# Performance work log

Measured on AMD Instinct MI355X. Metric: run time of the kernel, lower is better.

The kernel has to match this reference:

```python
import jax, jax.numpy as jnp
import numpy as np

N, E, B = 20000, 320000, 64
NODE_DIM, HID, HEADS, L, EMB = 128, 256, 4, 3, 256
C = HID // HEADS
NEG_SLOPE = 0.2
LN_EPS = 1e-5


def setup_inputs() -> dict:
    key = jax.random.key(0)
    ks = jax.random.split(key, 12)
    inp = {
        'x': jax.random.normal(ks[0], (N, NODE_DIM), jnp.float32),
        'edge_index': jax.random.randint(ks[1], (2, E), 0, N, jnp.int32),
        'batch': ((jnp.arange(N, dtype=jnp.int32) * B) // N).astype(jnp.int32),
        'W_in': jax.random.normal(ks[2], (NODE_DIM, HID), jnp.float32) * 0.05,
        'b_in': jnp.zeros((HID,), jnp.float32),
        'cls_token': jax.random.normal(ks[3], (HID,), jnp.float32),
        'W_gat': jax.random.normal(ks[4], (L, HID, HID), jnp.float32) * 0.05,
        'att_src': jax.random.normal(ks[5], (L, HEADS, C), jnp.float32) * 0.1,
        'att_dst': jax.random.normal(ks[6], (L, HEADS, C), jnp.float32) * 0.1,
        'b_gat': jnp.zeros((L, HID), jnp.float32),
        'ln_g': jnp.ones((L, HID), jnp.float32),
        'ln_b': jnp.zeros((L, HID), jnp.float32),
        'W_out': jax.random.normal(ks[7], (HID, EMB), jnp.float32) * 0.05,
        'b_out': jnp.zeros((EMB,), jnp.float32),
    }
    return inp


def _layer_norm(h, g, b):
    mu = jnp.mean(h, axis=-1, keepdims=True)
    var = jnp.mean(jnp.square(h - mu), axis=-1, keepdims=True)
    return (h - mu) * jax.lax.rsqrt(var + LN_EPS) * g + b


def _gat_layer(h, src, dst, n_nodes, W, a_s, a_d, bias):
    # PyG GATConv: shared linear, per-head attention, softmax over incoming edges
    xs = (h @ W).reshape(n_nodes, HEADS, C)          # (N',H,C)
    al_s = jnp.sum(xs * a_s, axis=-1)                # (N',H)
    al_d = jnp.sum(xs * a_d, axis=-1)                # (N',H)
    e = jax.nn.leaky_relu(al_s[src] + al_d[dst], NEG_SLOPE)  # (E',H)
    m = jax.ops.segment_max(e, dst, num_segments=n_nodes)
    ex = jnp.exp(e - m[dst])
    den = jax.ops.segment_sum(ex, dst, num_segments=n_nodes)
    alpha = ex / (den[dst] + 1e-16)                  # (E',H)
    msg = alpha[:, :, None] * xs[src]                # (E',H,C)
    out = jax.ops.segment_sum(msg, dst, num_segments=n_nodes)
    return out.reshape(n_nodes, HID) + bias


def reference(x, edge_index, batch, W_in, b_in, cls_token, W_gat, att_src,
              att_dst, b_gat, ln_g, ln_b, W_out, b_out):
    n_new = B + N
    h = x @ W_in + b_in                              # (N,HID)
    cls = jnp.broadcast_to(cls_token[None, :], (B, HID))
    h = jnp.concatenate([cls, h], axis=0)            # (B+N,HID)
    # build augmented edge list: shifted edges + bidirectional CLS edges + self loops
    src0 = edge_index[0] + B
    dst0 = edge_index[1] + B
    node_idx = jnp.arange(N, dtype=jnp.int32) + B
    cls_idx = batch
    loops = jnp.arange(n_new, dtype=jnp.int32)
    src = jnp.concatenate([src0, cls_idx, node_idx, loops])
    dst = jnp.concatenate([dst0, node_idx, cls_idx, loops])
    for l in range(L):
        g = _gat_layer(h, src, dst, n_new, W_gat[l], att_src[l], att_dst[l], b_gat[l])
        h = _layer_norm(h + g, ln_g[l], ln_b[l])
    z_e = h[:B] @ W_out + b_out                      # (B,EMB)
    return z_e
```

## Files before the change

kernel.cpp:

```cpp
#include <hip/hip_runtime.h>
#include <hip/hip_bf16.h>

constexpr int HID = 256;
constexpr int CAP = 64;
constexpr float NEG = 0.2f;
constexpr float EPS = 1e-5f;

typedef __attribute__((ext_vector_type(8))) short bf16x8;
typedef __attribute__((ext_vector_type(4))) float f32x4;

static __device__ __forceinline__ unsigned short f2bf(float f) {
    unsigned u = __builtin_bit_cast(unsigned, f);
    u += 0x7fffu + ((u >> 16) & 1u);
    return (unsigned short)(u >> 16);
}
static __device__ __forceinline__ float bf2f(unsigned short h) {
    return __builtin_bit_cast(float, ((unsigned)h) << 16);
}
static __device__ __forceinline__ float elk(float v) {
    v = v > 0.f ? v : NEG * v;
    return __expf(v);
}


__device__ __forceinline__ void frag_task(const float* __restrict__ W,
                                          ushort* __restrict__ out,
                                          int KS, int nmat, int q) {
    int per = KS * 1024;
    if (q >= per * nmat) return;
    int mat = q / per, r = q - mat * per;
    int l = r & 63, nf = (r >> 6) & 15, kk = r >> 10;
    const float* Wm = W + (size_t)mat * KS * 32 * 256;
    int kb = kk * 32 + ((l >> 4) << 3);
    int col = nf * 16 + (l & 15);
    bf16x8 v;
#pragma unroll
    for (int j = 0; j < 8; ++j) v[j] = (short)f2bf(Wm[(size_t)(kb + j) * 256 + col]);
    *(bf16x8*)(out + (size_t)q * 8) = v;
}

__global__ void k_pre(const float* __restrict__ x, ushort* __restrict__ xb,
                      const float* __restrict__ cls, ushort* __restrict__ h0,
                      const float* __restrict__ W_in, ushort* __restrict__ wf_in,
                      const float* __restrict__ W_gat, ushort* __restrict__ wf_gat,
                      const int* __restrict__ batch, int* lo, int* hi,
                      int* cursor, int* csr, int N, int B, int n_new) {
    int bid = blockIdx.x, t = threadIdx.x;
    const int nb_cvt  = (N * 128 / 4 + 255) / 256;
    const int nb_init = (n_new + 255) / 256;
    const int nb_csr  = (n_new * CAP + 255) / 256;
    const int nb_bnd  = (N + 255) / 256;
    const int nb_cls  = (B * HID / 4 + 255) / 256;
    const int nb_fin  = (4 * 1024 + 255) / 256;

    if (bid < nb_cvt) {
        int i = bid * 256 + t;
        int n4 = N * 128 / 4;
        if (i < n4) {
            float4 v = ((const float4*)x)[i];
            ushort4 o;
            o.x = f2bf(v.x); o.y = f2bf(v.y); o.z = f2bf(v.z); o.w = f2bf(v.w);
            ((ushort4*)xb)[i] = o;
        }
        return;
    }
    bid -= nb_cvt;
    if (bid < nb_init) {
        int i = bid * 256 + t;
        if (i < n_new) cursor[i] = 0;
        return;
    }
    bid -= nb_init;
    if (bid < nb_csr) {
        int i = bid * 256 + t;
        if (i < n_new * CAP) csr[i] = -1;
        return;
    }
    bid -= nb_csr;
    if (bid < nb_bnd) {
        int i = bid * 256 + t;
        if (i < N) {
            int b = batch[i];
            if (i == 0 || batch[i - 1] != b) lo[b] = i;
            if (i == N - 1 || batch[i + 1] != b) hi[b] = i + 1;
        }
        return;
    }
    bid -= nb_bnd;
    if (bid < nb_cls) {
        int i = bid * 256 + t;
        if (i < B * HID / 4) {
            int ch = (i & 63) * 4;
            ushort4 o;
            o.x = f2bf(cls[ch]); o.y = f2bf(cls[ch + 1]);
            o.z = f2bf(cls[ch + 2]); o.w = f2bf(cls[ch + 3]);
            ((ushort4*)h0)[i] = o;
        }
        return;
    }
    bid -= nb_cls;
    if (bid < nb_fin) {
        frag_task(W_in, wf_in, 4, 1, bid * 256 + t);
        return;
    }
    bid -= nb_fin;
    frag_task(W_gat, wf_gat, 8, 3, bid * 256 + t);
}


__global__ void k_fill(const int* __restrict__ src0, const int* __restrict__ dst0,
                       int* cursor, int* __restrict__ csr, int E, int B) {
    int e = blockIdx.x * blockDim.x + threadIdx.x;
    if (e < E) {
        int d = dst0[e] + B;
        int p = atomicAdd(&cursor[d], 1);
        if (p < CAP) csr[d * CAP + p] = src0[e] + B;
    }
}


__global__ void k_alpha(const int* __restrict__ csr, const int* __restrict__ cursor,
                        const float* __restrict__ als, const float* __restrict__ ald,
                        const int* __restrict__ batch,
                        float* __restrict__ a4T, float* __restrict__ acls,
                        float* __restrict__ aself, float* __restrict__ aclsinT,
                        int n_new, int B) {
    const int NSLOT = n_new * CAP;
    int i = blockIdx.x * 256 + threadIdx.x;
    if (i < NSLOT) {
        int d = i >> 6, p = i & (CAP - 1);
        int deg = cursor[d];
        deg = deg < CAP ? deg : CAP;
        int degp = (deg + 7) & ~7;
        if (p >= degp) return;
        int s = csr[i];
        float ox = 0.f, oy = 0.f, oz = 0.f, ow = 0.f;
        if (s >= 0) {
            float4 s4 = ((const float4*)als)[s];
            float4 d4 = ((const float4*)ald)[d];
            ox = elk(s4.x + d4.x);
            oy = elk(s4.y + d4.y);
            oz = elk(s4.z + d4.z);
            ow = elk(s4.w + d4.w);
        }
        a4T[i] = ox;
        a4T[(size_t)NSLOT + i] = oy;
        a4T[(size_t)2 * NSLOT + i] = oz;
        a4T[(size_t)3 * NSLOT + i] = ow;
        return;
    }
    int n = i - NSLOT;
    if (n < n_new) {
        float4 d4 = ((const float4*)ald)[n];
        float4 s4 = ((const float4*)als)[n];
        float4 o;
        o.x = elk(s4.x + d4.x);
        o.y = elk(s4.y + d4.y);
        o.z = elk(s4.z + d4.z);
        o.w = elk(s4.w + d4.w);
        ((float4*)aself)[n] = o;
        if (n >= B) {
            int c = batch[n - B];
            float4 cs = ((const float4*)als)[c];
            float4 p4;
            p4.x = elk(cs.x + d4.x);
            p4.y = elk(cs.y + d4.y);
            p4.z = elk(cs.z + d4.z);
            p4.w = elk(cs.w + d4.w);
            ((float4*)acls)[n] = p4;
            float4 cd = ((const float4*)ald)[c];
            aclsinT[n] = elk(s4.x + cd.x);
            aclsinT[(size_t)n_new + n] = elk(s4.y + cd.y);
            aclsinT[(size_t)2 * n_new + n] = elk(s4.z + cd.z);
            aclsinT[(size_t)3 * n_new + n] = elk(s4.w + cd.w);
        }
    }
}


template <int KS, bool ATT, bool BIAS>
__global__ __launch_bounds__(256, 4) void k_mgemm(
    const ushort* __restrict__ A, const ushort* __restrict__ Wf,
    const float* __restrict__ bias, ushort* __restrict__ outb,
    const float* __restrict__ att_s, const float* __restrict__ att_d,
    float* __restrict__ al_s, float* __restrict__ al_d, int rows)
{
    constexpr int K = KS * 32;
    int lane = threadIdx.x & 63, w = threadIdx.x >> 6;
    int rbase = blockIdx.x * 32;
    int arow0 = rbase + (lane & 15);
    int kofs = (lane >> 4) << 3;

    f32x4 acc[2][4];
#pragma unroll
    for (int mf = 0; mf < 2; ++mf)
#pragma unroll
        for (int nf = 0; nf < 4; ++nf) acc[mf][nf] = (f32x4){0.f, 0.f, 0.f, 0.f};

    const ushort* a0p = A + (size_t)arow0 * K + kofs;
    const ushort* a1p = a0p + (size_t)16 * K;
    bool g0 = arow0 < rows, g1 = (arow0 + 16) < rows;

#pragma unroll
    for (int kk = 0; kk < KS; ++kk) {
        bf16x8 af0 = {0, 0, 0, 0, 0, 0, 0, 0}, af1 = {0, 0, 0, 0, 0, 0, 0, 0};
        if (g0) af0 = *(const bf16x8*)(a0p + kk * 32);
        if (g1) af1 = *(const bf16x8*)(a1p + kk * 32);
        const bf16x8* wp = ((const bf16x8*)Wf) + (size_t)(kk * 16 + 4 * w) * 64 + lane;
#pragma unroll
        for (int nf = 0; nf < 4; ++nf) {
            bf16x8 bv = wp[nf * 64];
            acc[0][nf] = __builtin_amdgcn_mfma_f32_16x16x32_bf16(af0, bv, acc[0][nf], 0, 0, 0);
            acc[1][nf] = __builtin_amdgcn_mfma_f32_16x16x32_bf16(af1, bv, acc[1][nf], 0, 0, 0);
        }
    }

    int rg = (lane >> 4) * 4;
    int c0 = lane & 15;
    int colbase = w * 64;
    float bv[4];
    if (BIAS) {
#pragma unroll
        for (int nf = 0; nf < 4; ++nf) bv[nf] = bias[colbase + nf * 16 + c0];
    }
#pragma unroll
    for (int mf = 0; mf < 2; ++mf)
#pragma unroll
        for (int r = 0; r < 4; ++r) {
            int row = rbase + mf * 16 + rg + r;
            if (row < rows) {
#pragma unroll
                for (int nf = 0; nf < 4; ++nf) {
                    float v = acc[mf][nf][r];
                    if (BIAS) v += bv[nf];
                    outb[(size_t)row * HID + colbase + nf * 16 + c0] = f2bf(v);
                }
            }
        }

    if (ATT) {
        float as[4], ad[4];
#pragma unroll
        for (int nf = 0; nf < 4; ++nf) {
            as[nf] = att_s[colbase + nf * 16 + c0];
            ad[nf] = att_d[colbase + nf * 16 + c0];
        }
#pragma unroll
        for (int mf = 0; mf < 2; ++mf)
#pragma unroll
            for (int r = 0; r < 4; ++r) {
                float ps = 0.f, pd = 0.f;
#pragma unroll
                for (int nf = 0; nf < 4; ++nf) {
                    float v = acc[mf][nf][r];
                    ps += v * as[nf];
                    pd += v * ad[nf];
                }
#pragma unroll
                for (int o = 1; o < 16; o <<= 1) {
                    ps += __shfl_xor(ps, o, 64);
                    pd += __shfl_xor(pd, o, 64);
                }
                int row = rbase + mf * 16 + rg + r;
                if (c0 == 0 && row < rows) {
                    al_s[row * 4 + w] = ps;
                    al_d[row * 4 + w] = pd;
                }
            }
    }
}


__global__ __launch_bounds__(256, 4) void k_agg(
    const ushort* __restrict__ hb, const ushort* __restrict__ xs,
    const float* __restrict__ a4T, const float* __restrict__ acls,
    const float* __restrict__ aself, const float* __restrict__ aclsinT,
    const int* __restrict__ cursor, const int* __restrict__ csr,
    const int* __restrict__ batch, const int* __restrict__ lo,
    const int* __restrict__ hi,
    const float* __restrict__ b_gat, const float* __restrict__ ln_g,
    const float* __restrict__ ln_b,
    ushort* __restrict__ h_out, int n_new, int B)
{
    int t = threadIdx.x, w = t >> 6, lane = t & 63;
    int n = blockIdx.x * 4 + w;
    if (n >= n_new) return;
    int es = lane >> 5, cg = lane & 31, head = cg >> 3;
    const int NSLOT = n_new * CAP;

    float acc[8] = {0.f, 0.f, 0.f, 0.f, 0.f, 0.f, 0.f, 0.f};
    float den = 0.f;

    if (n >= B) {
        int gdeg = cursor[n];
        gdeg = gdeg < CAP ? gdeg : CAP;
        int gdegp = (gdeg + 7) & ~7;
        int clssrc = batch[n - B];
        bf16x8 xcls  = *((const bf16x8*)(xs + (size_t)clssrc * HID) + cg);
        bf16x8 xself = *((const bf16x8*)(xs + (size_t)n * HID) + cg);
        float acl = acls[n * 4 + head];
        float asf = aself[n * 4 + head];

        const int4* cp = (const int4*)(csr + n * CAP);
        const float4* ap = (const float4*)(a4T + (size_t)head * NSLOT + (size_t)n * CAP);
#pragma unroll 2
        for (int eb = 0; eb < gdegp; eb += 8) {
            int idx = (eb >> 2) + es;
            int4 s4 = cp[idx];
            float4 av = ap[idx];
            int s0 = s4.x < 0 ? 0 : s4.x;
            int s1 = s4.y < 0 ? 0 : s4.y;
            int s2 = s4.z < 0 ? 0 : s4.z;
            int s3 = s4.w < 0 ? 0 : s4.w;
            bf16x8 x0 = *((const bf16x8*)(xs + (size_t)s0 * HID) + cg);
            bf16x8 x1 = *((const bf16x8*)(xs + (size_t)s1 * HID) + cg);
            bf16x8 x2 = *((const bf16x8*)(xs + (size_t)s2 * HID) + cg);
            bf16x8 x3 = *((const bf16x8*)(xs + (size_t)s3 * HID) + cg);
            den += av.x + av.y + av.z + av.w;
#pragma unroll
            for (int j = 0; j < 8; ++j) {
                acc[j] += av.x * bf2f((unsigned short)x0[j]);
                acc[j] += av.y * bf2f((unsigned short)x1[j]);
                acc[j] += av.z * bf2f((unsigned short)x2[j]);
                acc[j] += av.w * bf2f((unsigned short)x3[j]);
            }
        }
        if (es == 0) {
            den += acl + asf;
#pragma unroll
            for (int j = 0; j < 8; ++j)
                acc[j] += acl * bf2f((unsigned short)xcls[j]) +
                          asf * bf2f((unsigned short)xself[j]);
        }
    } else {
        int cb = B + lo[n], cdeg = hi[n] - lo[n];
        bf16x8 xself = *((const bf16x8*)(xs + (size_t)n * HID) + cg);
        float asf = aself[n * 4 + head];
        const float* wp = aclsinT + (size_t)head * n_new;
        for (int eb = 0; eb < cdeg; eb += 8) {
            int b0 = eb + es * 4;
#pragma unroll
            for (int k = 0; k < 4; ++k) {
                int e = b0 + k;
                int ec = e < cdeg ? e : cdeg - 1;
                int src = cb + ec;
                float a = e < cdeg ? wp[src] : 0.f;
                bf16x8 xv = *((const bf16x8*)(xs + (size_t)src * HID) + cg);
                den += a;
#pragma unroll
                for (int j = 0; j < 8; ++j) acc[j] += a * bf2f((unsigned short)xv[j]);
            }
        }
        if (es == 0) {
            den += asf;
#pragma unroll
            for (int j = 0; j < 8; ++j) acc[j] += asf * bf2f((unsigned short)xself[j]);
        }
    }

#pragma unroll
    for (int j = 0; j < 8; ++j) acc[j] += __shfl_xor(acc[j], 32, 64);
    den += __shfl_xor(den, 32, 64);
    float inv = 1.f / (den + 1e-16f);

    bf16x8 hv = *((const bf16x8*)(hb + (size_t)n * HID) + cg);
    const float4* bgp = (const float4*)(b_gat + cg * 8);
    float4 bg0 = bgp[0], bg1 = bgp[1];
    float bg[8] = {bg0.x, bg0.y, bg0.z, bg0.w, bg1.x, bg1.y, bg1.z, bg1.w};
    float r[8];
#pragma unroll
    for (int j = 0; j < 8; ++j)
        r[j] = bf2f((unsigned short)hv[j]) + acc[j] * inv + bg[j];

    float ss = 0.f;
#pragma unroll
    for (int j = 0; j < 8; ++j) ss += r[j];
#pragma unroll
    for (int o = 1; o < 32; o <<= 1) ss += __shfl_xor(ss, o, 64);
    float mu = ss * (1.f / HID);
    float vv = 0.f;
#pragma unroll
    for (int j = 0; j < 8; ++j) { r[j] -= mu; vv += r[j] * r[j]; }
#pragma unroll
    for (int o = 1; o < 32; o <<= 1) vv += __shfl_xor(vv, o, 64);
    float rs = rsqrtf(vv * (1.f / HID) + EPS);

    if (es == 0) {
        const float4* gp = (const float4*)(ln_g + cg * 8);
        const float4* bp = (const float4*)(ln_b + cg * 8);
        float4 g0 = gp[0], g1 = gp[1];
        float4 lb0 = bp[0], lb1 = bp[1];
        float gg[8] = {g0.x, g0.y, g0.z, g0.w, g1.x, g1.y, g1.z, g1.w};
        float bb[8] = {lb0.x, lb0.y, lb0.z, lb0.w, lb1.x, lb1.y, lb1.z, lb1.w};
        bf16x8 o8;
#pragma unroll
        for (int j = 0; j < 8; ++j) o8[j] = (short)f2bf(r[j] * rs * gg[j] + bb[j]);
        *((bf16x8*)(h_out + (size_t)n * HID) + cg) = o8;
    }
}


__global__ __launch_bounds__(256) void k_clsfused(
    const ushort* __restrict__ hb, const ushort* __restrict__ xs,
    const float* __restrict__ als, const float* __restrict__ ald,
    const int* __restrict__ lo, const int* __restrict__ hi,
    const float* __restrict__ b_gat, const float* __restrict__ ln_g,
    const float* __restrict__ ln_b,
    const float* __restrict__ W_out, const float* __restrict__ b_out,
    float* __restrict__ z, int n_new, int B)
{
    __shared__ float sacc[4][256];
    __shared__ float sden[4][4];
    __shared__ float red[8];
    __shared__ float hs[256];
    int b = blockIdx.x;
    int t = threadIdx.x, w = t >> 6, lane = t & 63;
    int es = lane >> 5, cg = lane & 31, head = cg >> 3;

    int cb = B + lo[b], cdeg = hi[b] - lo[b];
    float ald_h = ald[b * 4 + head];

    float acc[8] = {0.f, 0.f, 0.f, 0.f, 0.f, 0.f, 0.f, 0.f};
    float den = 0.f;
    for (int eb = w * 8; eb < cdeg; eb += 32) {
        int b0 = eb + es * 4;
#pragma unroll
        for (int k = 0; k < 4; ++k) {
            int e = b0 + k;
            int ec = e < cdeg ? e : cdeg - 1;
            int src = cb + ec;
            float a = e < cdeg ? elk(als[src * 4 + head] + ald_h) : 0.f;
            bf16x8 xv = *((const bf16x8*)(xs + (size_t)src * HID) + cg);
            den += a;
#pragma unroll
            for (int j = 0; j < 8; ++j) acc[j] += a * bf2f((unsigned short)xv[j]);
        }
    }
#pragma unroll
    for (int j = 0; j < 8; ++j) acc[j] += __shfl_xor(acc[j], 32, 64);
    den += __shfl_xor(den, 32, 64);
    if (es == 0) {
#pragma unroll
        for (int j = 0; j < 8; ++j) sacc[w][cg * 8 + j] = acc[j];
        if ((cg & 7) == 0) sden[w][head] = den;
    }
    __syncthreads();

    int c = t, hh = c >> 6;
    float atot = sacc[0][c] + sacc[1][c] + sacc[2][c] + sacc[3][c];
    float dtot = sden[0][hh] + sden[1][hh] + sden[2][hh] + sden[3][hh];
    float asf = elk(als[b * 4 + hh] + ald[b * 4 + hh]);
    atot += asf * bf2f(xs[(size_t)b * HID + c]);
    dtot += asf;
    float r = bf2f(hb[(size_t)b * HID + c]) + atot / (dtot + 1e-16f) + b_gat[c];

    float s1 = r;
#pragma unroll
    for (int o = 32; o > 0; o >>= 1) s1 += __shfl_xor(s1, o, 64);
    if (lane == 0) red[w] = s1;
    __syncthreads();
    float mu = (red[0] + red[1] + red[2] + red[3]) * (1.f / HID);
    float d = r - mu;
    float v2 = d * d;
#pragma unroll
    for (int o = 32; o > 0; o >>= 1) v2 += __shfl_xor(v2, o, 64);
    if (lane == 0) red[4 + w] = v2;
    __syncthreads();
    float var = (red[4] + red[5] + red[6] + red[7]) * (1.f / HID);
    float rs = rsqrtf(var + EPS);
    hs[c] = d * rs * ln_g[c] + ln_b[c];
    __syncthreads();

    float o = b_out[t];
#pragma unroll 8
    for (int k = 0; k < HID; ++k) o += hs[k] * W_out[k * HID + t];
    z[(size_t)b * HID + t] = o;
}


extern "C" void kernel_launch(void* const* d_in, const int* in_sizes, int n_in,
                              void* d_out, int out_size, void* d_ws, size_t ws_size,
                              hipStream_t stream) {
    const float* x      = (const float*)d_in[0];
    const int*   ei     = (const int*)d_in[1];
    const int*   batch  = (const int*)d_in[2];
    const float* W_in   = (const float*)d_in[3];
    const float* b_in   = (const float*)d_in[4];
    const float* cls    = (const float*)d_in[5];
    const float* W_gat  = (const float*)d_in[6];
    const float* att_s  = (const float*)d_in[7];
    const float* att_d  = (const float*)d_in[8];
    const float* b_gat  = (const float*)d_in[9];
    const float* ln_g   = (const float*)d_in[10];
    const float* ln_b   = (const float*)d_in[11];
    const float* W_out  = (const float*)d_in[12];
    const float* b_out  = (const float*)d_in[13];

    const int N = in_sizes[0] / 128;
    const int E = in_sizes[1] / 2;
    const int B = 64;
    const int n_new = N + B;
    const int* src0 = ei;
    const int* dst0 = ei + E;

    char* p = (char*)d_ws;
    auto alloc = [&](size_t bytes) -> void* {
        void* r = (void*)p;
        p += (bytes + 255) & ~(size_t)255;
        return r;
    };
    int*    cursor = (int*)alloc((size_t)n_new * 4);
    int*    csr    = (int*)alloc((size_t)n_new * CAP * 4);
    int*    lo     = (int*)alloc((size_t)B * 4);
    int*    hi     = (int*)alloc((size_t)B * 4);
    ushort* xb     = (ushort*)alloc((size_t)N * 128 * 2);
    ushort* h0b    = (ushort*)alloc((size_t)n_new * HID * 2);
    ushort* h1b    = (ushort*)alloc((size_t)n_new * HID * 2);
    ushort* xsb    = (ushort*)alloc((size_t)n_new * HID * 2);
    float*  als    = (float*)alloc((size_t)n_new * 4 * 4);
    float*  aldv   = (float*)alloc((size_t)n_new * 4 * 4);
    float*  a4T    = (float*)alloc((size_t)n_new * CAP * 4 * 4);
    float*  acls   = (float*)alloc((size_t)n_new * 4 * 4);
    float*  aselfv = (float*)alloc((size_t)n_new * 4 * 4);
    float*  aclsinT= (float*)alloc((size_t)n_new * 4 * 4);
    ushort* wf_in  = (ushort*)alloc((size_t)4 * 1024 * 8 * 2);
    ushort* wf_gat = (ushort*)alloc((size_t)3 * 8 * 1024 * 8 * 2);

    const int nb_pre = (N * 128 / 4 + 255) / 256 + (n_new + 255) / 256 +
                       (n_new * CAP + 255) / 256 + (N + 255) / 256 +
                       (B * HID / 4 + 255) / 256 +
                       (4 * 1024 + 255) / 256 + (3 * 8 * 1024 + 255) / 256;
    k_pre<<<nb_pre, 256, 0, stream>>>(x, xb, cls, h0b, W_in, wf_in, W_gat, wf_gat,
                                      batch, lo, hi, cursor, csr, N, B, n_new);
    k_fill<<<(E + 255) / 256, 256, 0, stream>>>(src0, dst0, cursor, csr, E, B);

    k_mgemm<4, false, true><<<(N + 31) / 32, 256, 0, stream>>>(
        xb, wf_in, b_in, h0b + (size_t)B * HID, nullptr, nullptr, nullptr, nullptr, N);

    const int nb_alpha = (n_new * CAP + n_new + 255) / 256;
    ushort* cur = h0b;
    ushort* nxt = h1b;
    for (int l = 0; l < 2; ++l) {
        k_mgemm<8, true, false><<<(n_new + 31) / 32, 256, 0, stream>>>(
            cur, wf_gat + (size_t)l * 65536, nullptr, xsb,
            att_s + l * HID, att_d + l * HID, als, aldv, n_new);
        k_alpha<<<nb_alpha, 256, 0, stream>>>(
            csr, cursor, als, aldv, batch, a4T, acls, aselfv, aclsinT, n_new, B);
        k_agg<<<(n_new + 3) / 4, 256, 0, stream>>>(
            cur, xsb, a4T, acls, aselfv, aclsinT, cursor, csr, batch, lo, hi,
            b_gat + l * HID, ln_g + l * HID, ln_b + l * HID, nxt, n_new, B);
        ushort* tmp = cur; cur = nxt; nxt = tmp;
    }
    k_mgemm<8, true, false><<<(n_new + 31) / 32, 256, 0, stream>>>(
        cur, wf_gat + (size_t)2 * 65536, nullptr, xsb,
        att_s + 2 * HID, att_d + 2 * HID, als, aldv, n_new);
    k_clsfused<<<B, 256, 0, stream>>>(
        cur, xsb, als, aldv, lo, hi,
        b_gat + 2 * HID, ln_g + 2 * HID, ln_b + 2 * HID,
        W_out, b_out, (float*)d_out, n_new, B);
}
```

Baseline: 195.7 us.

## Fuse attention-coefficient computation into aggregation kernel and drop alpha buffers

Removes the separate k_alpha kernel and its large per-slot a4T buffer, plus the acls, aself and aclsinT buffers. Edge attention weights are now computed inside k_agg. Each wave stages its node's neighbour coefficients in a per-wave LDS array, and the CLS, self and CLS-incoming coefficients are computed inline. This avoids writing and re-reading tens of MB of coefficients per layer and saves one launch per layer. In exchange, k_agg does redundant exponentials on the CLS path, and correctness relies on LDS visibility within a single wave without a barrier.

```diff
diff --git a/kernel.cpp b/kernel.cpp
--- a/kernel.cpp
+++ b/kernel.cpp
@@ -119,65 +119,6 @@
 }
 
 
-__global__ void k_alpha(const int* __restrict__ csr, const int* __restrict__ cursor,
-                        const float* __restrict__ als, const float* __restrict__ ald,
-                        const int* __restrict__ batch,
-                        float* __restrict__ a4T, float* __restrict__ acls,
-                        float* __restrict__ aself, float* __restrict__ aclsinT,
-                        int n_new, int B) {
-    const int NSLOT = n_new * CAP;
-    int i = blockIdx.x * 256 + threadIdx.x;
-    if (i < NSLOT) {
-        int d = i >> 6, p = i & (CAP - 1);
-        int deg = cursor[d];
-        deg = deg < CAP ? deg : CAP;
-        int degp = (deg + 7) & ~7;
-        if (p >= degp) return;
-        int s = csr[i];
-        float ox = 0.f, oy = 0.f, oz = 0.f, ow = 0.f;
-        if (s >= 0) {
-            float4 s4 = ((const float4*)als)[s];
-            float4 d4 = ((const float4*)ald)[d];
-            ox = elk(s4.x + d4.x);
-            oy = elk(s4.y + d4.y);
-            oz = elk(s4.z + d4.z);
-            ow = elk(s4.w + d4.w);
-        }
-        a4T[i] = ox;
-        a4T[(size_t)NSLOT + i] = oy;
-        a4T[(size_t)2 * NSLOT + i] = oz;
-        a4T[(size_t)3 * NSLOT + i] = ow;
-        return;
-    }
-    int n = i - NSLOT;
-    if (n < n_new) {
-        float4 d4 = ((const float4*)ald)[n];
-        float4 s4 = ((const float4*)als)[n];
-        float4 o;
-        o.x = elk(s4.x + d4.x);
-        o.y = elk(s4.y + d4.y);
-        o.z = elk(s4.z + d4.z);
-        o.w = elk(s4.w + d4.w);
-        ((float4*)aself)[n] = o;
-        if (n >= B) {
-            int c = batch[n - B];
-            float4 cs = ((const float4*)als)[c];
-            float4 p4;
-            p4.x = elk(cs.x + d4.x);
-            p4.y = elk(cs.y + d4.y);
-            p4.z = elk(cs.z + d4.z);
-            p4.w = elk(cs.w + d4.w);
-            ((float4*)acls)[n] = p4;
-            float4 cd = ((const float4*)ald)[c];
-            aclsinT[n] = elk(s4.x + cd.x);
-            aclsinT[(size_t)n_new + n] = elk(s4.y + cd.y);
-            aclsinT[(size_t)2 * n_new + n] = elk(s4.z + cd.z);
-            aclsinT[(size_t)3 * n_new + n] = elk(s4.w + cd.w);
-        }
-    }
-}
-
-
 template <int KS, bool ATT, bool BIAS>
 __global__ __launch_bounds__(256, 4) void k_mgemm(
     const ushort* __restrict__ A, const ushort* __restrict__ Wf,
@@ -273,8 +214,7 @@
 
 __global__ __launch_bounds__(256, 4) void k_agg(
     const ushort* __restrict__ hb, const ushort* __restrict__ xs,
-    const float* __restrict__ a4T, const float* __restrict__ acls,
-    const float* __restrict__ aself, const float* __restrict__ aclsinT,
+    const float* __restrict__ als, const float* __restrict__ ald,
     const int* __restrict__ cursor, const int* __restrict__ csr,
     const int* __restrict__ batch, const int* __restrict__ lo,
     const int* __restrict__ hi,
@@ -282,11 +222,11 @@
     const float* __restrict__ ln_b,
     ushort* __restrict__ h_out, int n_new, int B)
 {
+    __shared__ float s_a[4][4][68];
     int t = threadIdx.x, w = t >> 6, lane = t & 63;
     int n = blockIdx.x * 4 + w;
     if (n >= n_new) return;
     int es = lane >> 5, cg = lane & 31, head = cg >> 3;
-    const int NSLOT = n_new * CAP;
 
     float acc[8] = {0.f, 0.f, 0.f, 0.f, 0.f, 0.f, 0.f, 0.f};
     float den = 0.f;
@@ -295,19 +235,33 @@
         int gdeg = cursor[n];
         gdeg = gdeg < CAP ? gdeg : CAP;
         int gdegp = (gdeg + 7) & ~7;
+        float4 ald4 = ((const float4*)ald)[n];
+        float ald_h = head == 0 ? ald4.x : head == 1 ? ald4.y : head == 2 ? ald4.z : ald4.w;
+
+        {
+            bool v = lane < gdeg;
+            int s = v ? csr[n * CAP + lane] : 0;
+            float4 sa = {0.f, 0.f, 0.f, 0.f};
+            if (v) sa = ((const float4*)als)[s];
+            s_a[w][0][lane] = v ? elk(sa.x + ald4.x) : 0.f;
+            s_a[w][1][lane] = v ? elk(sa.y + ald4.y) : 0.f;
+            s_a[w][2][lane] = v ? elk(sa.z + ald4.z) : 0.f;
+            s_a[w][3][lane] = v ? elk(sa.w + ald4.w) : 0.f;
+        }
+
         int clssrc = batch[n - B];
         bf16x8 xcls  = *((const bf16x8*)(xs + (size_t)clssrc * HID) + cg);
         bf16x8 xself = *((const bf16x8*)(xs + (size_t)n * HID) + cg);
-        float acl = acls[n * 4 + head];
-        float asf = aself[n * 4 + head];
+        float acl = elk(als[clssrc * 4 + head] + ald_h);
+        float asf = elk(als[n * 4 + head] + ald_h);
 
         const int4* cp = (const int4*)(csr + n * CAP);
-        const float4* ap = (const float4*)(a4T + (size_t)head * NSLOT + (size_t)n * CAP);
+        const float* apl = &s_a[w][head][0];
 #pragma unroll 2
         for (int eb = 0; eb < gdegp; eb += 8) {
             int idx = (eb >> 2) + es;
             int4 s4 = cp[idx];
-            float4 av = ap[idx];
+            float4 av = *(const float4*)(apl + idx * 4);
             int s0 = s4.x < 0 ? 0 : s4.x;
             int s1 = s4.y < 0 ? 0 : s4.y;
             int s2 = s4.z < 0 ? 0 : s4.z;
@@ -334,9 +288,9 @@
         }
     } else {
         int cb = B + lo[n], cdeg = hi[n] - lo[n];
+        float ald_h = ald[n * 4 + head];
         bf16x8 xself = *((const bf16x8*)(xs + (size_t)n * HID) + cg);
-        float asf = aself[n * 4 + head];
-        const float* wp = aclsinT + (size_t)head * n_new;
+        float asf = elk(als[n * 4 + head] + ald_h);
         for (int eb = 0; eb < cdeg; eb += 8) {
             int b0 = eb + es * 4;
 #pragma unroll
@@ -344,7 +298,7 @@
                 int e = b0 + k;
                 int ec = e < cdeg ? e : cdeg - 1;
                 int src = cb + ec;
-                float a = e < cdeg ? wp[src] : 0.f;
+                float a = e < cdeg ? elk(als[src * 4 + head] + ald_h) : 0.f;
                 bf16x8 xv = *((const bf16x8*)(xs + (size_t)src * HID) + cg);
                 den += a;
 #pragma unroll
@@ -519,10 +473,6 @@
     ushort* xsb    = (ushort*)alloc((size_t)n_new * HID * 2);
     float*  als    = (float*)alloc((size_t)n_new * 4 * 4);
     float*  aldv   = (float*)alloc((size_t)n_new * 4 * 4);
-    float*  a4T    = (float*)alloc((size_t)n_new * CAP * 4 * 4);
-    float*  acls   = (float*)alloc((size_t)n_new * 4 * 4);
-    float*  aselfv = (float*)alloc((size_t)n_new * 4 * 4);
-    float*  aclsinT= (float*)alloc((size_t)n_new * 4 * 4);
     ushort* wf_in  = (ushort*)alloc((size_t)4 * 1024 * 8 * 2);
     ushort* wf_gat = (ushort*)alloc((size_t)3 * 8 * 1024 * 8 * 2);
 
@@ -537,17 +487,14 @@
     k_mgemm<4, false, true><<<(N + 31) / 32, 256, 0, stream>>>(
         xb, wf_in, b_in, h0b + (size_t)B * HID, nullptr, nullptr, nullptr, nullptr, N);
 
-    const int nb_alpha = (n_new * CAP + n_new + 255) / 256;
     ushort* cur = h0b;
     ushort* nxt = h1b;
     for (int l = 0; l < 2; ++l) {
         k_mgemm<8, true, false><<<(n_new + 31) / 32, 256, 0, stream>>>(
             cur, wf_gat + (size_t)l * 65536, nullptr, xsb,
             att_s + l * HID, att_d + l * HID, als, aldv, n_new);
-        k_alpha<<<nb_alpha, 256, 0, stream>>>(
-            csr, cursor, als, aldv, batch, a4T, acls, aselfv, aclsinT, n_new, B);
         k_agg<<<(n_new + 3) / 4, 256, 0, stream>>>(
-            cur, xsb, a4T, acls, aselfv, aclsinT, cursor, csr, batch, lo, hi,
+            cur, xsb, als, aldv, cursor, csr, batch, lo, hi,
             b_gat + l * HID, ln_g + l * HID, ln_b + l * HID, nxt, n_new, B);
         ushort* tmp = cur; cur = nxt; nxt = tmp;
     }
```

Result: slower. 272.8 us (+39.4%).
